# Kernel tuning notes

Measured on AMD Instinct MI355X. Metric: run time of the kernel, lower is better.

## Reference

```python
import jax, jax.numpy as jnp
import numpy as np

H, ND, RD, VD = 16, 128, 64, 128  # heads, nope/rope/v head dims
EPS = 1e-6


def rmsnorm(x, g):
    return x * jax.lax.rsqrt(jnp.mean(x * x, axis=-1, keepdims=True) + EPS) * g


def apply_rope(x, cos, sin):
    # x: [B,T,h,D]; cos/sin: [1,T,1,D/2]; interleaved pair rotation
    x1, x2 = x[..., 0::2], x[..., 1::2]
    o1 = x1 * cos - x2 * sin
    o2 = x1 * sin + x2 * cos
    return jnp.stack([o1, o2], axis=-1).reshape(x.shape)


def setup_inputs() -> dict:
    key = jax.random.key(0)
    ks = jax.random.split(key, 10)
    B, T, D = 2, 2048, 2048
    QR, KVR = 1536, 512
    s = 0.02
    return {
        "x": jax.random.normal(ks[0], (B, T, D), jnp.float32),
        "w_cq": jax.random.normal(ks[1], (D, QR), jnp.float32) * s,
        "g_q": jnp.ones((QR,), jnp.float32),
        "w_ckv": jax.random.normal(ks[2], (D, KVR), jnp.float32) * s,
        "g_kv": jnp.ones((KVR,), jnp.float32),
        "w_dq_nope": jax.random.normal(ks[3], (QR, H * ND), jnp.float32) * s,
        "w_dq_rope": jax.random.normal(ks[4], (QR, H * RD), jnp.float32) * s,
        "w_dk_nope": jax.random.normal(ks[5], (KVR, H * ND), jnp.float32) * s,
        "w_dv": jax.random.normal(ks[6], (KVR, H * VD), jnp.float32) * s,
        "w_k_rope": jax.random.normal(ks[7], (D, RD), jnp.float32) * s,
        "w_out": jax.random.normal(ks[8], (H * VD, D), jnp.float32) * s,
    }


def reference(x, w_cq, g_q, w_ckv, g_kv, w_dq_nope, w_dq_rope,
              w_dk_nope, w_dv, w_k_rope, w_out):
    B, T, D = x.shape
    # low-rank latents + RMSNorm
    q_lat = rmsnorm(x @ w_cq, g_q)          # [B,T,QR]
    kv_lat = rmsnorm(x @ w_ckv, g_kv)        # [B,T,KVR]
    q_nope = (q_lat @ w_dq_nope).reshape(B, T, H, ND)
    q_rope = (q_lat @ w_dq_rope).reshape(B, T, H, RD)
    k_nope = (kv_lat @ w_dk_nope).reshape(B, T, H, ND)
    v = (kv_lat @ w_dv).reshape(B, T, H, VD)
    k_rope = (x @ w_k_rope).reshape(B, T, 1, RD)  # shared across heads
    # RoPE (start_pos = 0, no past_kv)
    pos = jnp.arange(T, dtype=jnp.float32)
    inv_freq = 1.0 / (10000.0 ** (jnp.arange(0, RD, 2, dtype=jnp.float32) / RD))
    ang = pos[:, None] * inv_freq[None, :]               # [T, RD/2]
    cos = jnp.cos(ang)[None, :, None, :]
    sin = jnp.sin(ang)[None, :, None, :]
    q_rope = apply_rope(q_rope, cos, sin)
    k_rope = apply_rope(k_rope, cos, sin)
    k_rope = jnp.broadcast_to(k_rope, (B, T, H, RD))
    q = jnp.concatenate([q_nope, q_rope], axis=-1).transpose(0, 2, 1, 3)  # [B,H,T,ND+RD]
    k = jnp.concatenate([k_nope, k_rope], axis=-1).transpose(0, 2, 1, 3)
    v_t = v.transpose(0, 2, 1, 3)                                        # [B,H,T,VD]
    # causal SDPA, scale = 1/sqrt(head_dim)
    scale = 1.0 / jnp.sqrt(jnp.asarray(ND + RD, jnp.float32))
    scores = jnp.einsum('bhqd,bhkd->bhqk', q, k) * scale
    causal = jnp.tril(jnp.ones((T, T), dtype=bool))
    scores = jnp.where(causal[None, None], scores, -jnp.inf)
    attn = jax.nn.softmax(scores, axis=-1)
    out = jnp.einsum('bhqk,bhkd->bhqd', attn, v_t)
    out = out.transpose(0, 2, 1, 3).reshape(B, T, H * VD) @ w_out        # [B,T,D]
    return out, k, v_t
```

## Files before the change

kernel.cpp:

```cpp
#include <hip/hip_runtime.h>
#include <cstdint>
#include <cstddef>

typedef _Float16 HT;
typedef _Float16 h8 __attribute__((ext_vector_type(8)));
typedef _Float16 h4 __attribute__((ext_vector_type(4)));
typedef float f32x4 __attribute__((ext_vector_type(4)));

constexpr int Tn  = 2048;
constexpr int Dm  = 2048;
constexpr int Hh  = 16;
constexpr int RDc = 64;
constexpr int QRc = 1536;
constexpr int KVRc= 512;
constexpr int BT  = 4096;

#define VWAIT(N) asm volatile("s_waitcnt vmcnt(" #N ")" ::: "memory")
#define SBAR()   __builtin_amdgcn_s_barrier()

__device__ __forceinline__ f32x4 mfma16(h8 a, h8 b, f32x4 c) {
    return __builtin_amdgcn_mfma_f32_16x16x32_f16(a, b, c, 0, 0, 0);
}
__device__ __forceinline__ void gload_lds16(const void* g, void* l) {
    __builtin_amdgcn_global_load_lds(
        (const __attribute__((address_space(1))) unsigned int*)g,
        (__attribute__((address_space(3))) unsigned int*)l, 16, 0, 0);
}

__global__ __launch_bounds__(256)
void cstab_kernel(float2* __restrict__ cs)
{
    const int idx = blockIdx.x * 256 + threadIdx.x;
    const int t = idx >> 5, i = idx & 31;
    const float ang = (float)t * exp2f(-(float)i * (13.287712379549449f / 32.f));
    cs[idx] = make_float2(cosf(ang), sinf(ang));
}

struct WT8 {
    const float* s[8];
    HT* d[8];
    int K[8], N[8], start[8];
};

__global__ __launch_bounds__(256)
void wtrans8_kernel(WT8 p)
{
    __shared__ float Ts[64][65];
    int seg = 0;
    #pragma unroll
    for (int i = 1; i < 8; i++) if ((int)blockIdx.x >= p.start[i]) seg = i;
    const float* src = p.s[seg];
    HT* dst = p.d[seg];
    const int K = p.K[seg], N = p.N[seg];
    const int bx = blockIdx.x - p.start[seg];
    const int nx = N >> 6;
    const int n0 = (bx % nx) * 64, k0 = (bx / nx) * 64;
    const int tid = threadIdx.x;
    {
        const int r = tid >> 2, c0 = (tid & 3) * 16;
        const float* s = src + (size_t)(k0 + r) * N + n0 + c0;
        #pragma unroll
        for (int j = 0; j < 4; j++)
            *reinterpret_cast<f32x4*>(&Ts[r][c0 + j * 4]) = *reinterpret_cast<const f32x4*>(s + j * 4);
    }
    __syncthreads();
    {
        const int c = tid >> 2, kq = (tid & 3) * 16;
        h8 o0, o1;
        #pragma unroll
        for (int j = 0; j < 8; j++) { o0[j] = (HT)Ts[kq + j][c]; o1[j] = (HT)Ts[kq + 8 + j][c]; }
        HT* d = dst + (size_t)(n0 + c) * K + k0 + kq;
        *reinterpret_cast<h8*>(d)     = o0;
        *reinterpret_cast<h8*>(d + 8) = o1;
    }
}

__global__ __launch_bounds__(256)
void convx_kernel(const float* __restrict__ x, HT* __restrict__ x16)
{
    const size_t i = ((size_t)blockIdx.x * 256 + threadIdx.x) * 8;
    f32x4 a = *reinterpret_cast<const f32x4*>(x + i);
    f32x4 b = *reinterpret_cast<const f32x4*>(x + i + 4);
    h8 v;
    #pragma unroll
    for (int j = 0; j < 4; j++) { v[j] = (HT)a[j]; v[4 + j] = (HT)b[j]; }
    *reinterpret_cast<h8*>(x16 + i) = v;
}

template<int EPI>
__global__ __launch_bounds__(256)
void gemm16d(const HT* __restrict__ A, const HT* __restrict__ Bt, const int K,
             HT* __restrict__ o1, HT* __restrict__ o2, HT* __restrict__ o3,
             float* __restrict__ f1, float* __restrict__ f2,
             const float2* __restrict__ cstab)
{
    __shared__ HT As[2][4096];
    __shared__ HT Bs[2][4096];

    const int tid  = threadIdx.x;
    const int lane = tid & 63;
    const int l15  = lane & 15, l4 = lane >> 4;
    const int w    = tid >> 6;
    const int wr   = w >> 1, wc = w & 1;
    const int m0   = blockIdx.y * 128;
    const int n0   = blockIdx.x * 128;

    f32x4 acc[4][4] = {};
    const int nk = K >> 5;

    const int schunk = ((lane & 3) ^ ((lane >> 2) & 3) ^ ((lane >> 4) & 3)) * 8;

#define GSTAGE(as_, bs_, kt_) do {                                             \
    _Pragma("unroll")                                                          \
    for (int i_ = 0; i_ < 2; i_++) {                                           \
        const int row_ = (w * 2 + i_) * 16 + (lane >> 2);                      \
        gload_lds16(A  + (size_t)(m0 + row_) * K + (kt_) + schunk,             \
                    (as_) + (w * 2 + i_) * 512);                               \
        gload_lds16(Bt + (size_t)(n0 + row_) * K + (kt_) + schunk,             \
                    (bs_) + (w * 2 + i_) * 512);                               \
    } } while (0)

    GSTAGE(As[0], Bs[0], 0);

    const int sl = (l4 ^ (l15 & 3) ^ ((l15 >> 2) & 3)) * 8;

    for (int kt = 0; kt < nk; kt++) {
        HT* as = As[kt & 1];
        HT* bs = Bs[kt & 1];
        if (kt + 1 < nk) {
            GSTAGE(As[(kt + 1) & 1], Bs[(kt + 1) & 1], (kt + 1) * 32);
            VWAIT(4);
        } else {
            VWAIT(0);
        }
        SBAR();

        h8 af[4], bf[4];
        #pragma unroll
        for (int f = 0; f < 4; f++)
            af[f] = *reinterpret_cast<const h8*>(&as[(wr * 64 + f * 16 + l15) * 32 + sl]);
        #pragma unroll
        for (int g = 0; g < 4; g++)
            bf[g] = *reinterpret_cast<const h8*>(&bs[(wc * 64 + g * 16 + l15) * 32 + sl]);
        #pragma unroll
        for (int f = 0; f < 4; f++)
            #pragma unroll
            for (int g = 0; g < 4; g++)
                acc[f][g] = mfma16(af[f], bf[g], acc[f][g]);
        SBAR();
    }
#undef GSTAGE

    #pragma unroll
    for (int f = 0; f < 4; f++) {
        #pragma unroll
        for (int g = 0; g < 4; g++) {
            const int row = m0 + wr * 64 + f * 16 + l4 * 4;
            const int col = n0 + wc * 64 + g * 16 + l15;
            if constexpr (EPI == 3) {
                #pragma unroll
                for (int r = 0; r < 4; r++)
                    f1[(size_t)(row + r) * 2048 + col] = acc[f][g][r];
            } else if constexpr (EPI == 0) {
                if (col < 1536) {
                    #pragma unroll
                    for (int r = 0; r < 4; r++)
                        o1[(size_t)(row + r) * 1536 + col] = (HT)acc[f][g][r];
                } else if (col < 2048) {
                    #pragma unroll
                    for (int r = 0; r < 4; r++)
                        o2[(size_t)(row + r) * 512 + (col - 1536)] = (HT)acc[f][g][r];
                } else if (col < 2112) {
                    const int cc = col - 2048;
                    const int i = cc >> 1;
                    const bool odd = cc & 1;
                    #pragma unroll
                    for (int r = 0; r < 4; r++) {
                        const int t = (row + r) & (Tn - 1);
                        const float2 cs = cstab[t * 32 + i];
                        const float v = acc[f][g][r];
                        const float p = __shfl_xor(v, 1);
                        const float ov = odd ? p * cs.y + v * cs.x : v * cs.x - p * cs.y;
                        o3[(size_t)(row + r) * 64 + cc] = (HT)ov;
                    }
                }
            } else if constexpr (EPI == 1) {
                if (col < 2048) {
                    #pragma unroll
                    for (int r = 0; r < 4; r++)
                        o1[(size_t)(row + r) * 2048 + col] = (HT)acc[f][g][r];
                } else {
                    const int cc = col - 2048;
                    const int i = (cc & 63) >> 1;
                    const bool odd = cc & 1;
                    #pragma unroll
                    for (int r = 0; r < 4; r++) {
                        const int t = (row + r) & (Tn - 1);
                        const float2 cs = cstab[t * 32 + i];
                        const float v = acc[f][g][r];
                        const float p = __shfl_xor(v, 1);
                        const float ov = odd ? p * cs.y + v * cs.x : v * cs.x - p * cs.y;
                        o2[(size_t)(row + r) * 1024 + cc] = (HT)ov;
                    }
                }
            } else {
                if (col < 2048) {
                    const int h = col >> 7, d = col & 127;
                    #pragma unroll
                    for (int r = 0; r < 4; r++) {
                        const int rw = row + r;
                        const int b = rw >> 11, t = rw & (Tn - 1);
                        o1[(size_t)rw * 2048 + col] = (HT)acc[f][g][r];
                        f1[((size_t)(b * Hh + h) * Tn + t) * 192 + d] = acc[f][g][r];
                    }
                } else {
                    const int c2 = col - 2048;
                    const int h = c2 >> 7, d = c2 & 127;
                    const int b = row >> 11, t0 = row & (Tn - 1);
                    h4 pk;
                    #pragma unroll
                    for (int r = 0; r < 4; r++) {
                        f2[((size_t)(b * Hh + h) * Tn + t0 + r) * 128 + d] = acc[f][g][r];
                        pk[r] = (HT)acc[f][g][r];
                    }
                    *reinterpret_cast<h4*>(&o3[((size_t)(b * Hh + h) * 128 + d) * Tn + t0]) = pk;
                }
            }
        }
    }
}

__global__ __launch_bounds__(256)
void kropebc_kernel(const HT* __restrict__ kr16, float* __restrict__ out_k)
{
    const int idx = blockIdx.x * 256 + threadIdx.x;
    const int j4 = (idx & 15) * 4;
    const int t  = (idx >> 4) & (Tn - 1);
    const int b  = idx >> 15;
    h4 v = *reinterpret_cast<const h4*>(&kr16[((size_t)(b * Tn + t)) * 64 + j4]);
    f32x4 f;
    #pragma unroll
    for (int r = 0; r < 4; r++) f[r] = (float)v[r];
    #pragma unroll
    for (int h = 0; h < Hh; h++)
        *reinterpret_cast<f32x4*>(&out_k[((size_t)(b * Hh + h) * Tn + t) * 192 + 128 + j4]) = f;
}

__global__ __launch_bounds__(256)
void rmsnorm2_kernel(HT* __restrict__ Xa, const float* __restrict__ ga,
                     HT* __restrict__ Xb, const float* __restrict__ gb)
{
    const int which = blockIdx.y;
    HT* X = which ? Xb : Xa;
    const float* g = which ? gb : ga;
    const int N = which ? 512 : 1536;
    const int row = blockIdx.x;
    HT* x = X + (size_t)row * N;
    float ss = 0.f;
    for (int i = threadIdx.x * 8; i < N; i += 2048) {
        h8 v = *reinterpret_cast<const h8*>(&x[i]);
        #pragma unroll
        for (int j = 0; j < 8; j++) { float f = (float)v[j]; ss += f * f; }
    }
    #pragma unroll
    for (int sh = 32; sh >= 1; sh >>= 1) ss += __shfl_xor(ss, sh);
    __shared__ float red[4];
    if ((threadIdx.x & 63) == 0) red[threadIdx.x >> 6] = ss;
    __syncthreads();
    const float tot = red[0] + red[1] + red[2] + red[3];
    const float scale = rsqrtf(tot / (float)N + 1e-6f);
    for (int i = threadIdx.x * 8; i < N; i += 2048) {
        h8 v = *reinterpret_cast<const h8*>(&x[i]);
        f32x4 g0 = *reinterpret_cast<const f32x4*>(&g[i]);
        f32x4 g1 = *reinterpret_cast<const f32x4*>(&g[i + 4]);
        #pragma unroll
        for (int j = 0; j < 4; j++) { v[j]   = (HT)((float)v[j]   * scale * g0[j]);
                                      v[4+j] = (HT)((float)v[4+j] * scale * g1[j]); }
        *reinterpret_cast<h8*>(&x[i]) = v;
    }
}

__global__ __launch_bounds__(256, 2)
void attn7_kernel(const HT* __restrict__ qn, const HT* __restrict__ qr,
                  const HT* __restrict__ kn, const HT* __restrict__ kr16,
                  const HT* __restrict__ vt, HT* __restrict__ ao)
{
    __shared__ HT Ks_n[64 * 128];
    __shared__ HT Vs[128 * 64];
    __shared__ HT Ps[4][32][72];

    const int tid  = threadIdx.x;
    const int lane = tid & 63;
    const int l15  = lane & 15, l4 = lane >> 4;
    const int w    = tid >> 6;

    const int bid = blockIdx.x;
    const int j   = bid >> 5;
    const int h   = bid & 15;
    const int b   = (bid >> 4) & 1;
    const int thi = 31 - j;

    const size_t bT = (size_t)b * Tn;
    const HT* vt_h = vt + ((size_t)(b * Hh + h) * 128) * Tn;
    const HT* krb  = kr16 + bT * 64;

    const int qw0 = j   * 64 + w * 16;
    const int qw1 = thi * 64 + w * 16;

    h8 aq0[6], aq1[6];
    {
        const size_t rq0 = bT + qw0 + l15;
        const HT* pn = qn + rq0 * 2048 + h * 128 + l4 * 8;
        #pragma unroll
        for (int f = 0; f < 4; f++) aq0[f] = *reinterpret_cast<const h8*>(pn + f * 32);
        const HT* pr = qr + rq0 * 1024 + h * 64 + l4 * 8;
        aq0[4] = *reinterpret_cast<const h8*>(pr);
        aq0[5] = *reinterpret_cast<const h8*>(pr + 32);
        const size_t rq1 = bT + qw1 + l15;
        const HT* pn1 = qn + rq1 * 2048 + h * 128 + l4 * 8;
        #pragma unroll
        for (int f = 0; f < 4; f++) aq1[f] = *reinterpret_cast<const h8*>(pn1 + f * 32);
        const HT* pr1 = qr + rq1 * 1024 + h * 64 + l4 * 8;
        aq1[4] = *reinterpret_cast<const h8*>(pr1);
        aq1[5] = *reinterpret_cast<const h8*>(pr1 + 32);
    }

    f32x4 o0[8] = {}, o1[8] = {};
    float m0v[4] = {-1e30f, -1e30f, -1e30f, -1e30f};
    float m1v[4] = {-1e30f, -1e30f, -1e30f, -1e30f};
    float l0v[4] = {0.f, 0.f, 0.f, 0.f};
    float l1v[4] = {0.f, 0.f, 0.f, 0.f};

    const float scl = 0.07216878364870323f;

#define SOFTMAX(sv, mv, lv, ov, qwx, prow)                                      \
{                                                                               \
    float al_[4];                                                               \
    _Pragma("unroll")                                                           \
    for (int r = 0; r < 4; r++) {                                               \
        const int qrow = (qwx) + l4 * 4 + r;                                    \
        float a_[4];                                                            \
        _Pragma("unroll")                                                       \
        for (int c = 0; c < 4; c++)                                             \
            a_[c] = (kb + c * 16 + l15 <= qrow) ? sv[c][r] * scl : -1e30f;      \
        float mx = fmaxf(fmaxf(a_[0], a_[1]), fmaxf(a_[2], a_[3]));             \
        _Pragma("unroll")                                                       \
        for (int sh = 1; sh < 16; sh <<= 1) mx = fmaxf(mx, __shfl_xor(mx, sh)); \
        const float mn = fmaxf(mv[r], mx);                                      \
        const float alpha = __expf(mv[r] - mn);                                 \
        mv[r] = mn;                                                             \
        float rs = 0.f;                                                         \
        _Pragma("unroll")                                                       \
        for (int c = 0; c < 4; c++) {                                           \
            const float e = __expf(a_[c] - mn);                                 \
            rs += e;                                                            \
            Ps[w][(prow) + l4 * 4 + r][c * 16 + l15] = (HT)e;                   \
        }                                                                       \
        _Pragma("unroll")                                                       \
        for (int sh = 1; sh < 16; sh <<= 1) rs += __shfl_xor(rs, sh);           \
        lv[r] = lv[r] * alpha + rs;                                             \
        al_[r] = alpha;                                                         \
    }                                                                           \
    _Pragma("unroll")                                                           \
    for (int g = 0; g < 8; g++)                                                 \
        _Pragma("unroll")                                                       \
        for (int r = 0; r < 4; r++) ov[g][r] *= al_[r];                         \
}

#define KBODY(ACT0)                                                             \
{                                                                               \
    f32x4 s0[4] = {}, s1[4] = {};                                               \
    __builtin_amdgcn_s_setprio(1);                                              \
    _Pragma("unroll")                                                           \
    for (int c = 0; c < 4; c++) {                                               \
        const int kr = c * 16 + l15;                                            \
        const HT* rp = krb + (size_t)(kb + kr) * 64 + l4 * 8;                   \
        const h8 br0 = *reinterpret_cast<const h8*>(rp);                        \
        const h8 br1 = *reinterpret_cast<const h8*>(rp + 32);                   \
        const int sw = (kr & 7) << 4;                                           \
        const char* kbase = (const char*)Ks_n + kr * 256;                       \
        _Pragma("unroll")                                                       \
        for (int f = 0; f < 4; f++) {                                           \
            const h8 kf = *(const h8*)(kbase + ((f * 64 + l4 * 16) ^ sw));      \
            s1[c] = mfma16(aq1[f], kf, s1[c]);                                  \
            if (ACT0) s0[c] = mfma16(aq0[f], kf, s0[c]);                        \
        }                                                                       \
        s1[c] = mfma16(aq1[4], br0, s1[c]);                                     \
        s1[c] = mfma16(aq1[5], br1, s1[c]);                                     \
        if (ACT0) { s0[c] = mfma16(aq0[4], br0, s0[c]);                         \
                    s0[c] = mfma16(aq0[5], br1, s0[c]); }                       \
    }                                                                           \
    __builtin_amdgcn_s_setprio(0);                                              \
    SOFTMAX(s1, m1v, l1v, o1, qw1, 16);                                         \
    if (ACT0) SOFTMAX(s0, m0v, l0v, o0, qw0, 0);                                \
    const h8 ap10 = *reinterpret_cast<const h8*>(&Ps[w][16 + l15][l4 * 8]);     \
    const h8 ap11 = *reinterpret_cast<const h8*>(&Ps[w][16 + l15][32 + l4 * 8]);\
    h8 ap00 = ap10, ap01 = ap11;                                                \
    if (ACT0) {                                                                 \
        ap00 = *reinterpret_cast<const h8*>(&Ps[w][l15][l4 * 8]);               \
        ap01 = *reinterpret_cast<const h8*>(&Ps[w][l15][32 + l4 * 8]);          \
    }                                                                           \
    __builtin_amdgcn_s_setprio(1);                                              \
    _Pragma("unroll")                                                           \
    for (int g = 0; g < 8; g++) {                                               \
        const int d = g * 16 + l15;                                             \
        const int sw = (d & 7) << 4;                                            \
        const char* vbase = (const char*)Vs + d * 128;                          \
        const h8 v0 = *(const h8*)(vbase + ((l4 * 16) ^ sw));                   \
        const h8 v1 = *(const h8*)(vbase + ((64 + l4 * 16) ^ sw));              \
        o1[g] = mfma16(ap10, v0, o1[g]);                                        \
        o1[g] = mfma16(ap11, v1, o1[g]);                                        \
        if (ACT0) { o0[g] = mfma16(ap00, v0, o0[g]);                            \
                    o0[g] = mfma16(ap01, v1, o0[g]); }                          \
    }                                                                           \
    __builtin_amdgcn_s_setprio(0);                                              \
}

    const int nkb = thi + 1;
    for (int kb64 = 0; kb64 < nkb; kb64++) {
        const int kb = kb64 * 64;
        __syncthreads();
        #pragma unroll
        for (int jj = 0; jj < 4; jj++) {
            const int r = (w * 4 + jj) * 4 + l4;
            const int cl = (l15 & 8) | ((l15 & 7) ^ (r & 7));
            gload_lds16(kn + (bT + kb + r) * 2048 + h * 128 + cl * 8,
                        &Ks_n[(w * 4 + jj) * 512]);
        }
        #pragma unroll
        for (int jj = 0; jj < 4; jj++) {
            const int d = (w * 4 + jj) * 8 + (lane >> 3);
            const int cl = (lane & 7) ^ (d & 7);
            gload_lds16(vt_h + (size_t)d * Tn + kb + cl * 8,
                        &Vs[(w * 4 + jj) * 512]);
        }
        __syncthreads();

        if (kb <= qw0 + 15) KBODY(1) else KBODY(0)
    }
#undef KBODY
#undef SOFTMAX

    {
        const size_t orow = bT + qw1 + l4 * 4;
        #pragma unroll
        for (int r = 0; r < 4; r++) {
            const float inv = 1.0f / l1v[r];
            HT* dst = ao + (orow + r) * 2048 + h * 128 + l15;
            #pragma unroll
            for (int g = 0; g < 8; g++) dst[g * 16] = (HT)(o1[g][r] * inv);
        }
    }
    {
        const size_t orow = bT + qw0 + l4 * 4;
        #pragma unroll
        for (int r = 0; r < 4; r++) {
            const float inv = 1.0f / l0v[r];
            HT* dst = ao + (orow + r) * 2048 + h * 128 + l15;
            #pragma unroll
            for (int g = 0; g < 8; g++) dst[g * 16] = (HT)(o0[g][r] * inv);
        }
    }
}

extern "C" void kernel_launch(void* const* d_in, const int* in_sizes, int n_in,
                              void* d_out, int out_size, void* d_ws, size_t ws_size,
                              hipStream_t stream)
{
    const float* x     = (const float*)d_in[0];
    const float* w_cq  = (const float*)d_in[1];
    const float* g_q   = (const float*)d_in[2];
    const float* w_ckv = (const float*)d_in[3];
    const float* g_kv  = (const float*)d_in[4];
    const float* w_dqn = (const float*)d_in[5];
    const float* w_dqr = (const float*)d_in[6];
    const float* w_dkn = (const float*)d_in[7];
    const float* w_dv  = (const float*)d_in[8];
    const float* w_kr  = (const float*)d_in[9];
    const float* w_out = (const float*)d_in[10];

    char* ws = (char*)d_ws;
    HT* cqT   = (HT*)(ws + 0);
    HT* ckvT  = (HT*)(ws + 6291456);
    HT* krT   = (HT*)(ws + 8388608);
    HT* dqnT  = (HT*)(ws + 8912896);
    HT* dqrT  = (HT*)(ws + 15204352);
    HT* dknT  = (HT*)(ws + 18350080);
    HT* dvT   = (HT*)(ws + 20447232);
    HT* outT  = (HT*)(ws + 22544384);
    HT* cq    = (HT*)(ws + 30932992);
    HT* ckv   = (HT*)(ws + 43515904);
    HT* qn    = (HT*)(ws + 47710208);
    HT* qr    = (HT*)(ws + 64487424);
    HT* kn    = (HT*)(ws + 72876032);
    HT* kr16  = (HT*)(ws + 89653248);
    HT* vt    = (HT*)(ws + 0);
    HT* x16   = qn;
    HT* ao    = qn;

    float* out_o = (float*)d_out;
    float* out_k = out_o + (size_t)BT * Dm;
    float* out_v = out_k + (size_t)2 * Hh * Tn * 192;
    float2* cstab = (float2*)out_v;

    const dim3 blk(256);

    cstab_kernel<<<dim3(256), blk, 0, stream>>>(cstab);

    WT8 wt;
    wt.s[0]=w_cq;  wt.d[0]=cqT;  wt.K[0]=2048; wt.N[0]=1536;
    wt.s[1]=w_ckv; wt.d[1]=ckvT; wt.K[1]=2048; wt.N[1]=512;
    wt.s[2]=w_kr;  wt.d[2]=krT;  wt.K[2]=2048; wt.N[2]=64;
    wt.s[3]=w_dqn; wt.d[3]=dqnT; wt.K[3]=1536; wt.N[3]=2048;
    wt.s[4]=w_dqr; wt.d[4]=dqrT; wt.K[4]=1536; wt.N[4]=1024;
    wt.s[5]=w_dkn; wt.d[5]=dknT; wt.K[5]=512;  wt.N[5]=2048;
    wt.s[6]=w_dv;  wt.d[6]=dvT;  wt.K[6]=512;  wt.N[6]=2048;
    wt.s[7]=w_out; wt.d[7]=outT; wt.K[7]=2048; wt.N[7]=2048;
    {
        int acc = 0;
        for (int i = 0; i < 8; i++) {
            wt.start[i] = acc;
            acc += (wt.N[i] >> 6) * (wt.K[i] >> 6);
        }
        wtrans8_kernel<<<dim3(acc), blk, 0, stream>>>(wt);
    }

    convx_kernel<<<dim3(4096), blk, 0, stream>>>(x, x16);

    gemm16d<0><<<dim3(17, BT/128), blk, 0, stream>>>(x16, cqT, Dm,
        cq, ckv, kr16, nullptr, nullptr, cstab);
    kropebc_kernel<<<dim3(256), blk, 0, stream>>>(kr16, out_k);

    rmsnorm2_kernel<<<dim3(BT, 2), blk, 0, stream>>>(cq, g_q, ckv, g_kv);

    gemm16d<1><<<dim3(24, BT/128), blk, 0, stream>>>(cq, dqnT, QRc,
        qn, qr, nullptr, nullptr, nullptr, cstab);
    gemm16d<2><<<dim3(32, BT/128), blk, 0, stream>>>(ckv, dknT, KVRc,
        kn, nullptr, vt, out_k, out_v, nullptr);

    attn7_kernel<<<dim3(512), blk, 0, stream>>>(qn, qr, kn, kr16, vt, ao);

    gemm16d<3><<<dim3(16, BT/128), blk, 0, stream>>>(ao, outT, Dm,
        nullptr, nullptr, nullptr, out_o, nullptr, nullptr);
}
```

Measured before the change: 357.8 us.

## Replace GEMM with 8-wave 256x128 tile and 4-slot LDS pipeline

The 256-thread 128x128 GEMM is replaced by a 512-thread kernel that computes a 256x128 tile, so each block reads B once for twice as many rows. K-steps of 32 are staged into a four-slot ring of 96KB dynamic LDS, with loads issued several phases ahead. MFMA work is raised in priority with s_setprio and fenced with sched_barrier so that loads and compute overlap. Larger tiles halve the grid along M, leaving fewer blocks to fill the CUs, and the bigger LDS footprint may limit how many blocks fit per CU.

After: 384.0 us, median of 2. 7.3% more time.

```diff
diff --git a/kernel.cpp b/kernel.cpp
--- a/kernel.cpp
+++ b/kernel.cpp
@@ -88,97 +88,114 @@
 }
 
 template<int EPI>
-__global__ __launch_bounds__(256)
-void gemm16d(const HT* __restrict__ A, const HT* __restrict__ Bt, const int K,
-             HT* __restrict__ o1, HT* __restrict__ o2, HT* __restrict__ o3,
-             float* __restrict__ f1, float* __restrict__ f2,
-             const float2* __restrict__ cstab)
-{
-    __shared__ HT As[2][4096];
-    __shared__ HT Bs[2][4096];
+__global__ __launch_bounds__(512, 2)
+void gemm8p(const HT* __restrict__ A, const HT* __restrict__ Bt, const int K,
+            HT* __restrict__ o1, HT* __restrict__ o2, HT* __restrict__ o3,
+            float* __restrict__ f1, float* __restrict__ f2,
+            const float2* __restrict__ cstab)
+{
+    extern __shared__ char smem[];
 
     const int tid  = threadIdx.x;
     const int lane = tid & 63;
     const int l15  = lane & 15, l4 = lane >> 4;
     const int w    = tid >> 6;
     const int wr   = w >> 1, wc = w & 1;
-    const int m0   = blockIdx.y * 128;
+    const int m0   = blockIdx.y * 256;
     const int n0   = blockIdx.x * 128;
 
     f32x4 acc[4][4] = {};
-    const int nk = K >> 5;
-
-    const int schunk = ((lane & 3) ^ ((lane >> 2) & 3) ^ ((lane >> 4) & 3)) * 8;
-
-#define GSTAGE(as_, bs_, kt_) do {                                             \
+    const int nk = K >> 6;
+
+    const int sch = (lane & 3) ^ ((lane >> 2) & 3) ^ ((lane >> 4) & 3);
+    const int swr = (l15 & 3) ^ ((l15 >> 2) & 3);
+
+    const int sarow = w * 32 + (lane >> 2);
+    const int sbrow = w * 16 + (lane >> 2);
+
+#define STAGE(slot_, srck_) do {                                               \
+    HT* stg_ = (HT*)(smem + (slot_) * 24576);                                  \
+    gload_lds16(A  + (size_t)(m0 + sarow)      * K + (srck_) + sch * 8,        \
+                stg_ + w * 1024);                                              \
+    gload_lds16(A  + (size_t)(m0 + sarow + 16) * K + (srck_) + sch * 8,        \
+                stg_ + w * 1024 + 512);                                        \
+    gload_lds16(Bt + (size_t)(n0 + sbrow)      * K + (srck_) + sch * 8,        \
+                stg_ + 8192 + w * 512);                                        \
+    } while (0)
+
+#define PHASE(cons_, stg_, srck_) do {                                         \
+    const char* sa_ = smem + (cons_) * 24576;                                  \
+    h8 af_[4], bf_[4];                                                         \
     _Pragma("unroll")                                                          \
-    for (int i_ = 0; i_ < 2; i_++) {                                           \
-        const int row_ = (w * 2 + i_) * 16 + (lane >> 2);                      \
-        gload_lds16(A  + (size_t)(m0 + row_) * K + (kt_) + schunk,             \
-                    (as_) + (w * 2 + i_) * 512);                               \
-        gload_lds16(Bt + (size_t)(n0 + row_) * K + (kt_) + schunk,             \
-                    (bs_) + (w * 2 + i_) * 512);                               \
-    } } while (0)
-
-    GSTAGE(As[0], Bs[0], 0);
-
-    const int sl = (l4 ^ (l15 & 3) ^ ((l15 >> 2) & 3)) * 8;
-
-    for (int kt = 0; kt < nk; kt++) {
-        HT* as = As[kt & 1];
-        HT* bs = Bs[kt & 1];
-        if (kt + 1 < nk) {
-            GSTAGE(As[(kt + 1) & 1], Bs[(kt + 1) & 1], (kt + 1) * 32);
-            VWAIT(4);
-        } else {
-            VWAIT(0);
-        }
-        SBAR();
-
-        h8 af[4], bf[4];
-        #pragma unroll
-        for (int f = 0; f < 4; f++)
-            af[f] = *reinterpret_cast<const h8*>(&as[(wr * 64 + f * 16 + l15) * 32 + sl]);
-        #pragma unroll
-        for (int g = 0; g < 4; g++)
-            bf[g] = *reinterpret_cast<const h8*>(&bs[(wc * 64 + g * 16 + l15) * 32 + sl]);
-        #pragma unroll
-        for (int f = 0; f < 4; f++)
-            #pragma unroll
-            for (int g = 0; g < 4; g++)
-                acc[f][g] = mfma16(af[f], bf[g], acc[f][g]);
-        SBAR();
-    }
-#undef GSTAGE
+    for (int i_ = 0; i_ < 4; i_++)                                             \
+        af_[i_] = *(const h8*)(sa_ + (wr * 64 + i_ * 16 + l15) * 64            \
+                                   + (l4 ^ swr) * 16);                         \
+    _Pragma("unroll")                                                          \
+    for (int j_ = 0; j_ < 4; j_++)                                             \
+        bf_[j_] = *(const h8*)(sa_ + 16384 + (wc * 64 + j_ * 16 + l15) * 64    \
+                                   + (l4 ^ swr) * 16);                         \
+    STAGE(stg_, srck_);                                                        \
+    VWAIT(6);                                                                  \
+    SBAR();                                                                    \
+    asm volatile("s_waitcnt lgkmcnt(0)" ::: "memory");                         \
+    __builtin_amdgcn_sched_barrier(0);                                         \
+    __builtin_amdgcn_s_setprio(1);                                             \
+    _Pragma("unroll")                                                          \
+    for (int i_ = 0; i_ < 4; i_++)                                             \
+        _Pragma("unroll")                                                      \
+        for (int j_ = 0; j_ < 4; j_++)                                         \
+            acc[i_][j_] = mfma16(af_[i_], bf_[j_], acc[i_][j_]);               \
+    __builtin_amdgcn_s_setprio(0);                                             \
+    SBAR();                                                                    \
+    } while (0)
+
+    STAGE(0, 0);
+    STAGE(1, 32);
+    STAGE(2, 64);
+    VWAIT(6);
+    SBAR();
+
+    for (int t = 0; t < nk; t++) {
+        const int s0 = (2 * t) & 3;
+        const int s1 = (2 * t + 1) & 3;
+        const int st0 = (2 * t + 3) & 3;
+        const int k1 = (t + 1 < nk ? t + 1 : nk - 1) * 64 + 32;
+        const int k2 = (t + 2 < nk ? t + 2 : nk - 1) * 64;
+        PHASE(s0, st0, k1);
+        PHASE(s1, s0,  k2);
+    }
+    VWAIT(0);
+#undef PHASE
+#undef STAGE
 
     #pragma unroll
-    for (int f = 0; f < 4; f++) {
-        #pragma unroll
-        for (int g = 0; g < 4; g++) {
-            const int row = m0 + wr * 64 + f * 16 + l4 * 4;
-            const int col = n0 + wc * 64 + g * 16 + l15;
+    for (int i = 0; i < 4; i++) {
+        #pragma unroll
+        for (int j = 0; j < 4; j++) {
+            const int row = m0 + wr * 64 + i * 16 + l4 * 4;
+            const int col = n0 + wc * 64 + j * 16 + l15;
             if constexpr (EPI == 3) {
                 #pragma unroll
                 for (int r = 0; r < 4; r++)
-                    f1[(size_t)(row + r) * 2048 + col] = acc[f][g][r];
+                    f1[(size_t)(row + r) * 2048 + col] = acc[i][j][r];
             } else if constexpr (EPI == 0) {
                 if (col < 1536) {
                     #pragma unroll
                     for (int r = 0; r < 4; r++)
-                        o1[(size_t)(row + r) * 1536 + col] = (HT)acc[f][g][r];
+                        o1[(size_t)(row + r) * 1536 + col] = (HT)acc[i][j][r];
                 } else if (col < 2048) {
                     #pragma unroll
                     for (int r = 0; r < 4; r++)
-                        o2[(size_t)(row + r) * 512 + (col - 1536)] = (HT)acc[f][g][r];
+                        o2[(size_t)(row + r) * 512 + (col - 1536)] = (HT)acc[i][j][r];
                 } else if (col < 2112) {
                     const int cc = col - 2048;
-                    const int i = cc >> 1;
+                    const int ii = cc >> 1;
                     const bool odd = cc & 1;
                     #pragma unroll
                     for (int r = 0; r < 4; r++) {
                         const int t = (row + r) & (Tn - 1);
-                        const float2 cs = cstab[t * 32 + i];
-                        const float v = acc[f][g][r];
+                        const float2 cs = cstab[t * 32 + ii];
+                        const float v = acc[i][j][r];
                         const float p = __shfl_xor(v, 1);
                         const float ov = odd ? p * cs.y + v * cs.x : v * cs.x - p * cs.y;
                         o3[(size_t)(row + r) * 64 + cc] = (HT)ov;
@@ -188,16 +205,16 @@
                 if (col < 2048) {
                     #pragma unroll
                     for (int r = 0; r < 4; r++)
-                        o1[(size_t)(row + r) * 2048 + col] = (HT)acc[f][g][r];
+                        o1[(size_t)(row + r) * 2048 + col] = (HT)acc[i][j][r];
                 } else {
                     const int cc = col - 2048;
-                    const int i = (cc & 63) >> 1;
+                    const int ii = (cc & 63) >> 1;
                     const bool odd = cc & 1;
                     #pragma unroll
                     for (int r = 0; r < 4; r++) {
                         const int t = (row + r) & (Tn - 1);
-                        const float2 cs = cstab[t * 32 + i];
-                        const float v = acc[f][g][r];
+                        const float2 cs = cstab[t * 32 + ii];
+                        const float v = acc[i][j][r];
                         const float p = __shfl_xor(v, 1);
                         const float ov = odd ? p * cs.y + v * cs.x : v * cs.x - p * cs.y;
                         o2[(size_t)(row + r) * 1024 + cc] = (HT)ov;
@@ -210,8 +227,8 @@
                     for (int r = 0; r < 4; r++) {
                         const int rw = row + r;
                         const int b = rw >> 11, t = rw & (Tn - 1);
-                        o1[(size_t)rw * 2048 + col] = (HT)acc[f][g][r];
-                        f1[((size_t)(b * Hh + h) * Tn + t) * 192 + d] = acc[f][g][r];
+                        o1[(size_t)rw * 2048 + col] = (HT)acc[i][j][r];
+                        f1[((size_t)(b * Hh + h) * Tn + t) * 192 + d] = acc[i][j][r];
                     }
                 } else {
                     const int c2 = col - 2048;
@@ -220,8 +237,8 @@
                     h4 pk;
                     #pragma unroll
                     for (int r = 0; r < 4; r++) {
-                        f2[((size_t)(b * Hh + h) * Tn + t0 + r) * 128 + d] = acc[f][g][r];
-                        pk[r] = (HT)acc[f][g][r];
+                        f2[((size_t)(b * Hh + h) * Tn + t0 + r) * 128 + d] = acc[i][j][r];
+                        pk[r] = (HT)acc[i][j][r];
                     }
                     *reinterpret_cast<h4*>(&o3[((size_t)(b * Hh + h) * 128 + d) * Tn + t0]) = pk;
                 }
@@ -504,6 +521,12 @@
     float2* cstab = (float2*)out_v;
 
     const dim3 blk(256);
+    const unsigned GEMM_LDS = 98304;
+
+    (void)hipFuncSetAttribute((const void*)gemm8p<0>, hipFuncAttributeMaxDynamicSharedMemorySize, (int)GEMM_LDS);
+    (void)hipFuncSetAttribute((const void*)gemm8p<1>, hipFuncAttributeMaxDynamicSharedMemorySize, (int)GEMM_LDS);
+    (void)hipFuncSetAttribute((const void*)gemm8p<2>, hipFuncAttributeMaxDynamicSharedMemorySize, (int)GEMM_LDS);
+    (void)hipFuncSetAttribute((const void*)gemm8p<3>, hipFuncAttributeMaxDynamicSharedMemorySize, (int)GEMM_LDS);
 
     cstab_kernel<<<dim3(256), blk, 0, stream>>>(cstab);
 
@@ -527,19 +550,19 @@
 
     convx_kernel<<<dim3(4096), blk, 0, stream>>>(x, x16);
 
-    gemm16d<0><<<dim3(17, BT/128), blk, 0, stream>>>(x16, cqT, Dm,
+    gemm8p<0><<<dim3(17, 16), dim3(512), GEMM_LDS, stream>>>(x16, cqT, Dm,
         cq, ckv, kr16, nullptr, nullptr, cstab);
     kropebc_kernel<<<dim3(256), blk, 0, stream>>>(kr16, out_k);
 
     rmsnorm2_kernel<<<dim3(BT, 2), blk, 0, stream>>>(cq, g_q, ckv, g_kv);
 
-    gemm16d<1><<<dim3(24, BT/128), blk, 0, stream>>>(cq, dqnT, QRc,
+    gemm8p<1><<<dim3(24, 16), dim3(512), GEMM_LDS, stream>>>(cq, dqnT, QRc,
         qn, qr, nullptr, nullptr, nullptr, cstab);
-    gemm16d<2><<<dim3(32, BT/128), blk, 0, stream>>>(ckv, dknT, KVRc,
+    gemm8p<2><<<dim3(32, 16), dim3(512), GEMM_LDS, stream>>>(ckv, dknT, KVRc,
         kn, nullptr, vt, out_k, out_v, nullptr);
 
     attn7_kernel<<<dim3(512), blk, 0, stream>>>(qn, qr, kn, kr16, vt, ao);
 
-    gemm16d<3><<<dim3(16, BT/128), blk, 0, stream>>>(ao, outT, Dm,
+    gemm8p<3><<<dim3(16, 16), dim3(512), GEMM_LDS, stream>>>(ao, outT, Dm,
         nullptr, nullptr, nullptr, out_o, nullptr, nullptr);
 }
```

## Triple-buffer GEMM LDS stages to drop second barrier; fuse k_rope broadcast into GEMM epilogue

Applied to the files above, without the earlier changes.

The GEMM now cycles through three LDS buffers instead of two. This lets it remove the trailing barrier in each k-iteration, since the buffer being overwritten is two stages behind the one being read. The separate k_rope broadcast kernel is removed: the first GEMM's epilogue now writes the rotated k_rope value directly into all 16 head slots of the fp32 k output. This saves one launch and a reread of kr16. The cost is more LDS per block, which may lower occupancy, and the epilogue now does scattered scalar stores instead of vectorized ones.

After: 402.8 us. 1.13x slower.

```diff
diff --git a/kernel.cpp b/kernel.cpp
--- a/kernel.cpp
+++ b/kernel.cpp
@@ -89,13 +89,13 @@
 
 template<int EPI>
 __global__ __launch_bounds__(256)
-void gemm16d(const HT* __restrict__ A, const HT* __restrict__ Bt, const int K,
+void gemm16r(const HT* __restrict__ A, const HT* __restrict__ Bt, const int K,
              HT* __restrict__ o1, HT* __restrict__ o2, HT* __restrict__ o3,
              float* __restrict__ f1, float* __restrict__ f2,
              const float2* __restrict__ cstab)
 {
-    __shared__ HT As[2][4096];
-    __shared__ HT Bs[2][4096];
+    __shared__ HT As[3][4096];
+    __shared__ HT Bs[3][4096];
 
     const int tid  = threadIdx.x;
     const int lane = tid & 63;
@@ -124,17 +124,19 @@
 
     const int sl = (l4 ^ (l15 & 3) ^ ((l15 >> 2) & 3)) * 8;
 
+    int cur = 0;
     for (int kt = 0; kt < nk; kt++) {
-        HT* as = As[kt & 1];
-        HT* bs = Bs[kt & 1];
+        int nxt = cur + 1; if (nxt == 3) nxt = 0;
         if (kt + 1 < nk) {
-            GSTAGE(As[(kt + 1) & 1], Bs[(kt + 1) & 1], (kt + 1) * 32);
+            GSTAGE(As[nxt], Bs[nxt], (kt + 1) * 32);
             VWAIT(4);
         } else {
             VWAIT(0);
         }
         SBAR();
 
+        const HT* as = As[cur];
+        const HT* bs = Bs[cur];
         h8 af[4], bf[4];
         #pragma unroll
         for (int f = 0; f < 4; f++)
@@ -147,7 +149,7 @@
             #pragma unroll
             for (int g = 0; g < 4; g++)
                 acc[f][g] = mfma16(af[f], bf[g], acc[f][g]);
-        SBAR();
+        cur = nxt;
     }
 #undef GSTAGE
 
@@ -176,12 +178,17 @@
                     const bool odd = cc & 1;
                     #pragma unroll
                     for (int r = 0; r < 4; r++) {
-                        const int t = (row + r) & (Tn - 1);
+                        const int rw = row + r;
+                        const int t = rw & (Tn - 1);
+                        const int b = rw >> 11;
                         const float2 cs = cstab[t * 32 + i];
                         const float v = acc[f][g][r];
                         const float p = __shfl_xor(v, 1);
                         const float ov = odd ? p * cs.y + v * cs.x : v * cs.x - p * cs.y;
-                        o3[(size_t)(row + r) * 64 + cc] = (HT)ov;
+                        o3[(size_t)rw * 64 + cc] = (HT)ov;
+                        #pragma unroll
+                        for (int h = 0; h < Hh; h++)
+                            f1[((size_t)(b * Hh + h) * Tn + t) * 192 + 128 + cc] = ov;
                     }
                 }
             } else if constexpr (EPI == 1) {
@@ -228,22 +235,6 @@
             }
         }
     }
-}
-
-__global__ __launch_bounds__(256)
-void kropebc_kernel(const HT* __restrict__ kr16, float* __restrict__ out_k)
-{
-    const int idx = blockIdx.x * 256 + threadIdx.x;
-    const int j4 = (idx & 15) * 4;
-    const int t  = (idx >> 4) & (Tn - 1);
-    const int b  = idx >> 15;
-    h4 v = *reinterpret_cast<const h4*>(&kr16[((size_t)(b * Tn + t)) * 64 + j4]);
-    f32x4 f;
-    #pragma unroll
-    for (int r = 0; r < 4; r++) f[r] = (float)v[r];
-    #pragma unroll
-    for (int h = 0; h < Hh; h++)
-        *reinterpret_cast<f32x4*>(&out_k[((size_t)(b * Hh + h) * Tn + t) * 192 + 128 + j4]) = f;
 }
 
 __global__ __launch_bounds__(256)
@@ -527,19 +518,18 @@
 
     convx_kernel<<<dim3(4096), blk, 0, stream>>>(x, x16);
 
-    gemm16d<0><<<dim3(17, BT/128), blk, 0, stream>>>(x16, cqT, Dm,
-        cq, ckv, kr16, nullptr, nullptr, cstab);
-    kropebc_kernel<<<dim3(256), blk, 0, stream>>>(kr16, out_k);
+    gemm16r<0><<<dim3(17, BT/128), blk, 0, stream>>>(x16, cqT, Dm,
+        cq, ckv, kr16, out_k, nullptr, cstab);
 
     rmsnorm2_kernel<<<dim3(BT, 2), blk, 0, stream>>>(cq, g_q, ckv, g_kv);
 
-    gemm16d<1><<<dim3(24, BT/128), blk, 0, stream>>>(cq, dqnT, QRc,
+    gemm16r<1><<<dim3(24, BT/128), blk, 0, stream>>>(cq, dqnT, QRc,
         qn, qr, nullptr, nullptr, nullptr, cstab);
-    gemm16d<2><<<dim3(32, BT/128), blk, 0, stream>>>(ckv, dknT, KVRc,
+    gemm16r<2><<<dim3(32, BT/128), blk, 0, stream>>>(ckv, dknT, KVRc,
         kn, nullptr, vt, out_k, out_v, nullptr);
 
     attn7_kernel<<<dim3(512), blk, 0, stream>>>(qn, qr, kn, kr16, vt, ao);
 
-    gemm16d<3><<<dim3(16, BT/128), blk, 0, stream>>>(ao, outT, Dm,
+    gemm16r<3><<<dim3(16, BT/128), blk, 0, stream>>>(ao, outT, Dm,
         nullptr, nullptr, nullptr, out_o, nullptr, nullptr);
 }
```

## Fold softmax scale into Q, use exp2, skip rescale with lazy max threshold

Applied to the files above, without the earlier changes.

Pre-multiplies Q fragments by the softmax scale times log2(e) so scores come out of the MFMA in base-2 units, and uses exp2 instead of expf. Adds a lazy-rescale path: when every row's new max stays within 8 of the running max across the wavefront, the max shuffle-reduction and O rescaling are skipped. Row sums are kept per lane and reduced only once at the end. This trims per-tile shuffles and ALU work in the softmax. The cost is an extra fp16 rounding of the scaled Q and partial sums that can grow by up to 2^8 relative to the stored max.

Result: faster. 346.9 us (-3.0%).

```diff
diff --git a/kernel.cpp b/kernel.cpp
--- a/kernel.cpp
+++ b/kernel.cpp
@@ -281,7 +281,7 @@
 }
 
 __global__ __launch_bounds__(256, 2)
-void attn7_kernel(const HT* __restrict__ qn, const HT* __restrict__ qr,
+void attn9_kernel(const HT* __restrict__ qn, const HT* __restrict__ qr,
                   const HT* __restrict__ kn, const HT* __restrict__ kr16,
                   const HT* __restrict__ vt, HT* __restrict__ ao)
 {
@@ -309,20 +309,21 @@
 
     h8 aq0[6], aq1[6];
     {
+        const HT sc = (HT)(0.07216878364870323f * 1.4426950408889634f);
         const size_t rq0 = bT + qw0 + l15;
         const HT* pn = qn + rq0 * 2048 + h * 128 + l4 * 8;
         #pragma unroll
-        for (int f = 0; f < 4; f++) aq0[f] = *reinterpret_cast<const h8*>(pn + f * 32);
+        for (int f = 0; f < 4; f++) aq0[f] = *reinterpret_cast<const h8*>(pn + f * 32) * sc;
         const HT* pr = qr + rq0 * 1024 + h * 64 + l4 * 8;
-        aq0[4] = *reinterpret_cast<const h8*>(pr);
-        aq0[5] = *reinterpret_cast<const h8*>(pr + 32);
+        aq0[4] = *reinterpret_cast<const h8*>(pr) * sc;
+        aq0[5] = *reinterpret_cast<const h8*>(pr + 32) * sc;
         const size_t rq1 = bT + qw1 + l15;
         const HT* pn1 = qn + rq1 * 2048 + h * 128 + l4 * 8;
         #pragma unroll
-        for (int f = 0; f < 4; f++) aq1[f] = *reinterpret_cast<const h8*>(pn1 + f * 32);
+        for (int f = 0; f < 4; f++) aq1[f] = *reinterpret_cast<const h8*>(pn1 + f * 32) * sc;
         const HT* pr1 = qr + rq1 * 1024 + h * 64 + l4 * 8;
-        aq1[4] = *reinterpret_cast<const h8*>(pr1);
-        aq1[5] = *reinterpret_cast<const h8*>(pr1 + 32);
+        aq1[4] = *reinterpret_cast<const h8*>(pr1) * sc;
+        aq1[5] = *reinterpret_cast<const h8*>(pr1 + 32) * sc;
     }
 
     f32x4 o0[8] = {}, o1[8] = {};
@@ -331,40 +332,54 @@
     float l0v[4] = {0.f, 0.f, 0.f, 0.f};
     float l1v[4] = {0.f, 0.f, 0.f, 0.f};
 
-    const float scl = 0.07216878364870323f;
-
-#define SOFTMAX(sv, mv, lv, ov, qwx, prow)                                      \
+#define SMX(sv, mv, lv, ov, qwx, prow)                                          \
 {                                                                               \
-    float al_[4];                                                               \
+    float a_[4][4]; float mxr_[4]; bool ok_ = true;                             \
     _Pragma("unroll")                                                           \
     for (int r = 0; r < 4; r++) {                                               \
         const int qrow = (qwx) + l4 * 4 + r;                                    \
-        float a_[4];                                                            \
         _Pragma("unroll")                                                       \
         for (int c = 0; c < 4; c++)                                             \
-            a_[c] = (kb + c * 16 + l15 <= qrow) ? sv[c][r] * scl : -1e30f;      \
-        float mx = fmaxf(fmaxf(a_[0], a_[1]), fmaxf(a_[2], a_[3]));             \
+            a_[r][c] = (kb + c * 16 + l15 <= qrow) ? sv[c][r] : -1e30f;         \
+        mxr_[r] = fmaxf(fmaxf(a_[r][0], a_[r][1]), fmaxf(a_[r][2], a_[r][3]));  \
+        ok_ = ok_ && (mxr_[r] <= mv[r] + 8.f);                                  \
+    }                                                                           \
+    if (__builtin_expect((bool)__all(ok_), 1)) {                                \
         _Pragma("unroll")                                                       \
-        for (int sh = 1; sh < 16; sh <<= 1) mx = fmaxf(mx, __shfl_xor(mx, sh)); \
-        const float mn = fmaxf(mv[r], mx);                                      \
-        const float alpha = __expf(mv[r] - mn);                                 \
-        mv[r] = mn;                                                             \
-        float rs = 0.f;                                                         \
+        for (int r = 0; r < 4; r++) {                                           \
+            float rs = 0.f;                                                     \
+            _Pragma("unroll")                                                   \
+            for (int c = 0; c < 4; c++) {                                       \
+                const float e = __builtin_exp2f(a_[r][c] - mv[r]);              \
+                rs += e;                                                        \
+                Ps[w][(prow) + l4 * 4 + r][c * 16 + l15] = (HT)e;               \
+            }                                                                   \
+            lv[r] += rs;                                                        \
+        }                                                                       \
+    } else {                                                                    \
+        float al_[4];                                                           \
         _Pragma("unroll")                                                       \
-        for (int c = 0; c < 4; c++) {                                           \
-            const float e = __expf(a_[c] - mn);                                 \
-            rs += e;                                                            \
-            Ps[w][(prow) + l4 * 4 + r][c * 16 + l15] = (HT)e;                   \
+        for (int r = 0; r < 4; r++) {                                           \
+            float mx = mxr_[r];                                                 \
+            _Pragma("unroll")                                                   \
+            for (int sh = 1; sh < 16; sh <<= 1) mx = fmaxf(mx, __shfl_xor(mx, sh)); \
+            const float mn = fmaxf(mv[r], mx);                                  \
+            al_[r] = __builtin_exp2f(mv[r] - mn);                               \
+            mv[r] = mn;                                                         \
+            float rs = 0.f;                                                     \
+            _Pragma("unroll")                                                   \
+            for (int c = 0; c < 4; c++) {                                       \
+                const float e = __builtin_exp2f(a_[r][c] - mn);                 \
+                rs += e;                                                        \
+                Ps[w][(prow) + l4 * 4 + r][c * 16 + l15] = (HT)e;               \
+            }                                                                   \
+            lv[r] = lv[r] * al_[r] + rs;                                        \
         }                                                                       \
         _Pragma("unroll")                                                       \
-        for (int sh = 1; sh < 16; sh <<= 1) rs += __shfl_xor(rs, sh);           \
-        lv[r] = lv[r] * alpha + rs;                                             \
-        al_[r] = alpha;                                                         \
+        for (int g = 0; g < 8; g++)                                             \
+            _Pragma("unroll")                                                   \
+            for (int r = 0; r < 4; r++) ov[g][r] *= al_[r];                     \
     }                                                                           \
-    _Pragma("unroll")                                                           \
-    for (int g = 0; g < 8; g++)                                                 \
-        _Pragma("unroll")                                                       \
-        for (int r = 0; r < 4; r++) ov[g][r] *= al_[r];                         \
 }
 
 #define KBODY(ACT0)                                                             \
@@ -391,8 +406,8 @@
                     s0[c] = mfma16(aq0[5], br1, s0[c]); }                       \
     }                                                                           \
     __builtin_amdgcn_s_setprio(0);                                              \
-    SOFTMAX(s1, m1v, l1v, o1, qw1, 16);                                         \
-    if (ACT0) SOFTMAX(s0, m0v, l0v, o0, qw0, 0);                                \
+    SMX(s1, m1v, l1v, o1, qw1, 16);                                             \
+    if (ACT0) SMX(s0, m0v, l0v, o0, qw0, 0);                                    \
     const h8 ap10 = *reinterpret_cast<const h8*>(&Ps[w][16 + l15][l4 * 8]);     \
     const h8 ap11 = *reinterpret_cast<const h8*>(&Ps[w][16 + l15][32 + l4 * 8]);\
     h8 ap00 = ap10, ap01 = ap11;                                                \
@@ -439,13 +454,16 @@
         if (kb <= qw0 + 15) KBODY(1) else KBODY(0)
     }
 #undef KBODY
-#undef SOFTMAX
+#undef SMX
 
     {
         const size_t orow = bT + qw1 + l4 * 4;
         #pragma unroll
         for (int r = 0; r < 4; r++) {
-            const float inv = 1.0f / l1v[r];
+            float rsum = l1v[r];
+            #pragma unroll
+            for (int sh = 1; sh < 16; sh <<= 1) rsum += __shfl_xor(rsum, sh);
+            const float inv = 1.0f / rsum;
             HT* dst = ao + (orow + r) * 2048 + h * 128 + l15;
             #pragma unroll
             for (int g = 0; g < 8; g++) dst[g * 16] = (HT)(o1[g][r] * inv);
@@ -455,7 +473,10 @@
         const size_t orow = bT + qw0 + l4 * 4;
         #pragma unroll
         for (int r = 0; r < 4; r++) {
-            const float inv = 1.0f / l0v[r];
+            float rsum = l0v[r];
+            #pragma unroll
+            for (int sh = 1; sh < 16; sh <<= 1) rsum += __shfl_xor(rsum, sh);
+            const float inv = 1.0f / rsum;
             HT* dst = ao + (orow + r) * 2048 + h * 128 + l15;
             #pragma unroll
             for (int g = 0; g < 8; g++) dst[g * 16] = (HT)(o0[g][r] * inv);
@@ -538,7 +559,7 @@
     gemm16d<2><<<dim3(32, BT/128), blk, 0, stream>>>(ckv, dknT, KVRc,
         kn, nullptr, vt, out_k, out_v, nullptr);
 
-    attn7_kernel<<<dim3(512), blk, 0, stream>>>(qn, qr, kn, kr16, vt, ao);
+    attn9_kernel<<<dim3(512), blk, 0, stream>>>(qn, qr, kn, kr16, vt, ao);
 
     gemm16d<3><<<dim3(16, BT/128), blk, 0, stream>>>(ao, outT, Dm,
         nullptr, nullptr, nullptr, out_o, nullptr, nullptr);
```
